# Performance work log

Hardware: AMD Instinct MI355X
Metric: run time of the kernel (lower is better)

The kernel has to match this reference:

```python
import jax, jax.numpy as jnp
import numpy as np

B, S, D, H = 8, 2048, 1024, 128  # batch, seq (== CONTEXT_WINDOW), embed dim, headspace


def setup_inputs() -> dict:
    key = jax.random.key(0)
    ks = jax.random.split(key, 7)
    scale = 1.0 / np.sqrt(D)
    return {
        "x": jax.random.normal(ks[0], (B, S, D), dtype=jnp.float32),
        "Wq": jax.random.normal(ks[1], (D, H), dtype=jnp.float32) * scale,
        "bq": jax.random.normal(ks[2], (H,), dtype=jnp.float32) * 0.01,
        "Wk": jax.random.normal(ks[3], (D, H), dtype=jnp.float32) * scale,
        "bk": jax.random.normal(ks[4], (H,), dtype=jnp.float32) * 0.01,
        "Wv": jax.random.normal(ks[5], (D, H), dtype=jnp.float32) * scale,
        "bv": jax.random.normal(ks[6], (H,), dtype=jnp.float32) * 0.01,
    }


def reference(x, Wq, bq, Wk, bk, Wv, bv):
    # x: [B, S, D]
    embedlen = x.shape[-1]
    q = x @ Wq + bq  # [B, S, H]
    k = x @ Wk + bk  # [B, S, H]
    v = x @ Wv + bv  # [B, S, H]
    # NOTE: original code MULTIPLIES by sqrt(embedlen) (embedlen = full embed dim) --
    # faithful reproduction of the source, not the standard 1/sqrt(head_dim).
    scale = jnp.sqrt(jnp.asarray(embedlen, dtype=x.dtype))
    scores = jnp.einsum("bsh,bth->bst", q, k) * scale  # [B, S, S]
    seqlen = x.shape[1]
    causal = jnp.tril(jnp.ones((seqlen, seqlen), dtype=bool))
    scores = jnp.where(causal, scores, -jnp.inf)
    attn = jax.nn.softmax(scores, axis=-1)
    return jnp.einsum("bst,bth->bsh", attn, v)  # [B, S, H]
```

## Files before the change

kernel.cpp:

```cpp
#include <hip/hip_runtime.h>
#include <math.h>

#define SEQ 2048
#define DIM 1024
#define HD  128
#define NB  8
#define M_TOT (NB * SEQ)

typedef __attribute__((ext_vector_type(8))) short   short8;
typedef __attribute__((ext_vector_type(4))) short   short4v;
typedef __attribute__((ext_vector_type(4))) float   floatx4;

__device__ __forceinline__ unsigned short f2bf(float f) {
    unsigned u = __builtin_bit_cast(unsigned, f);
    u += 0x7FFFu + ((u >> 16) & 1u);
    return (unsigned short)(u >> 16);
}
__device__ __forceinline__ float bf2f(unsigned short h) {
    unsigned u = ((unsigned)h) << 16;
    return __builtin_bit_cast(float, u);
}
__device__ __forceinline__ void async16(const void* g, void* l) {
    __builtin_amdgcn_global_load_lds(
        (const __attribute__((address_space(1))) unsigned int*)g,
        (__attribute__((address_space(3))) unsigned int*)l, 16, 0, 0);
}

#define MFMA16(a, b, c) __builtin_amdgcn_mfma_f32_16x16x32_bf16((a), (b), (c), 0, 0, 0)

__global__ __launch_bounds__(256) void wt_prep(
    const float* __restrict__ Wq, const float* __restrict__ Wk, const float* __restrict__ Wv,
    unsigned short* __restrict__ Wth, unsigned short* __restrict__ Wtl)
{
    int idx = blockIdx.x * 256 + threadIdx.x;
    int k   = idx & 1023;
    int n   = (idx >> 10) & 127;
    int mat = idx >> 17;
    const float* W = (mat == 0) ? Wq : (mat == 1) ? Wk : Wv;
    float v = W[k * HD + n];
    unsigned short hi = f2bf(v);
    Wth[idx] = hi;
    Wtl[idx] = f2bf(v - bf2f(hi));
}

__global__ __launch_bounds__(512, 4) void qkv_fused(
    const float* __restrict__ x,
    const unsigned short* __restrict__ Wth, const unsigned short* __restrict__ Wtl,
    const float* __restrict__ bq, const float* __restrict__ bk, const float* __restrict__ bv,
    unsigned short* __restrict__ Qh, unsigned short* __restrict__ Ql,
    unsigned short* __restrict__ Kh, unsigned short* __restrict__ Kl,
    unsigned short* __restrict__ Vt)
{
    __shared__ short lds[56 * 512];

    const int t    = threadIdx.x;
    const int lane = t & 63;
    const int w    = t >> 6;
    const int lrow = lane & 15;
    const int quad = lane >> 4;

    const int R0 = blockIdx.x * 64;
    const int z  = blockIdx.y;
    const int mh = w & 1;
    const int nh = w >> 1;

    auto stageB = [&](int k0, int qb) {
        #pragma unroll
        for (int i = 0; i < 3; ++i) {
            int f = i * 8 + w;
            if (f < 20) {
                int p   = (f >= 12);
                int ff  = p ? (f - 12) : f;
                int mat = ff >> 2, nfl = ff & 3;
                const unsigned short* src = (p ? Wtl : Wth) + (size_t)mat * (HD * DIM)
                    + (size_t)((z * 4 + nfl) * 16 + lrow) * DIM + k0 + quad * 8;
                async16(src, &lds[(qb * 28 + 8 + f) * 512 + lane * 8]);
            }
        }
    };

    const int arow = t >> 3;
    const int akk  = (t & 7) * 4;
    auto xload = [&](int k0) -> float4 {
        return *(const float4*)&x[(size_t)(R0 + arow) * DIM + k0 + akk];
    };
    auto stageA = [&](float4 xv, int qb) {
        float xf[4] = {xv.x, xv.y, xv.z, xv.w};
        short4v hv, lv;
        #pragma unroll
        for (int j = 0; j < 4; ++j) {
            unsigned short h = f2bf(xf[j]);
            hv[j] = (short)h;
            lv[j] = (short)f2bf(xf[j] - bf2f(h));
        }
        int mi = arow >> 4, lr = arow & 15, qd = akk >> 3, el = akk & 7;
        int base = (qb * 28 + mi * 2) * 512 + (qd * 16 + lr) * 8 + el;
        *(short4v*)&lds[base]       = hv;
        *(short4v*)&lds[base + 512] = lv;
    };

    floatx4 acc[2][3];
    const floatx4 zf = {0.f, 0.f, 0.f, 0.f};
    #pragma unroll
    for (int mi2 = 0; mi2 < 2; ++mi2)
        #pragma unroll
        for (int c = 0; c < 3; ++c) acc[mi2][c] = zf;

    auto compute = [&](int qb) {
        short8 a[2][2];
        #pragma unroll
        for (int mi2 = 0; mi2 < 2; ++mi2)
            #pragma unroll
            for (int p = 0; p < 2; ++p)
                a[mi2][p] = *(short8*)&lds[(qb * 28 + (mh * 2 + mi2) * 2 + p) * 512 + lane * 8];

        short8 bhq = *(short8*)&lds[(qb * 28 + 8 +  0 + nh) * 512 + lane * 8];
        short8 bhk = *(short8*)&lds[(qb * 28 + 8 +  4 + nh) * 512 + lane * 8];
        short8 bhv = *(short8*)&lds[(qb * 28 + 8 +  8 + nh) * 512 + lane * 8];
        short8 blq = *(short8*)&lds[(qb * 28 + 20 + 0 + nh) * 512 + lane * 8];
        short8 blk = *(short8*)&lds[(qb * 28 + 20 + 4 + nh) * 512 + lane * 8];

        #pragma unroll
        for (int mi2 = 0; mi2 < 2; ++mi2) {
            acc[mi2][0] = MFMA16(a[mi2][0], bhq, acc[mi2][0]);
            acc[mi2][1] = MFMA16(a[mi2][0], bhk, acc[mi2][1]);
            acc[mi2][2] = MFMA16(a[mi2][0], bhv, acc[mi2][2]);
            acc[mi2][0] = MFMA16(a[mi2][1], bhq, acc[mi2][0]);
            acc[mi2][1] = MFMA16(a[mi2][1], bhk, acc[mi2][1]);
            acc[mi2][0] = MFMA16(a[mi2][0], blq, acc[mi2][0]);
            acc[mi2][1] = MFMA16(a[mi2][0], blk, acc[mi2][1]);
        }
    };

    stageB(0, 0);
    stageA(xload(0), 0);
    float4 xn0 = xload(32);
    float4 xn1 = xload(64);

    for (int it = 0; it < 32; ++it) {
        __syncthreads();
        const int k0 = it * 32;
        const int q  = it & 1;

        if (it < 31) {
            stageB(k0 + 32, q ^ 1);
            stageA(xn0, q ^ 1);
            xn0 = xn1;
            int kx = (k0 + 96 <= DIM - 32) ? (k0 + 96) : (DIM - 32);
            xn1 = xload(kx);
        }

        compute(q);
    }

    const int col = (z * 4 + nh) * 16 + lrow;
    const float bqv = bq[col], bkv = bk[col], bvv = bv[col];
    #pragma unroll
    for (int mi2 = 0; mi2 < 2; ++mi2) {
        #pragma unroll
        for (int reg = 0; reg < 4; ++reg) {
            int gm = R0 + (mh * 2 + mi2) * 16 + quad * 4 + reg;
            float vq = (acc[mi2][0][reg] + bqv) * 32.0f;
            unsigned short h = f2bf(vq);
            Qh[(size_t)gm * HD + col] = h;
            Ql[(size_t)gm * HD + col] = f2bf(vq - bf2f(h));
            float vk = acc[mi2][1][reg] + bkv;
            h = f2bf(vk);
            Kh[(size_t)gm * HD + col] = h;
            Kl[(size_t)gm * HD + col] = f2bf(vk - bf2f(h));
            float vv = acc[mi2][2][reg] + bvv;
            int b = gm >> 11, s = gm & 2047;
            Vt[((size_t)b * HD + col) * SEQ + s] = f2bf(vv);
        }
    }
}

__global__ __launch_bounds__(256) void flash_attn(
    const unsigned short* __restrict__ Qh, const unsigned short* __restrict__ Ql,
    const unsigned short* __restrict__ Kh, const unsigned short* __restrict__ Kl,
    const unsigned short* __restrict__ Vt, float* __restrict__ out,
    float* __restrict__ Opart, float* __restrict__ ML, int split)
{
    __shared__ short lds[52 * 512];

    const int t    = threadIdx.x;
    const int lane = t & 63;
    const int w    = t >> 6;
    const int lrow = lane & 15;
    const int quad = lane >> 4;

    const int idx = blockIdx.x;
    const int b   = idx & 7;
    const int h   = split ? ((idx >> 3) & 1) : 0;
    const int s   = split ? (63 - (idx >> 4)) : (63 - (idx >> 3));
    const int T   = s + 1;
    const int Th  = (T + 1) >> 1;
    const int t0  = split ? (h ? Th : 0) : 0;
    const int t1  = split ? (h ? T : Th) : T;

    if (split && t0 >= t1) {
        float* op = Opart + (size_t)idx * 4096;
        for (int i = t; i < 4096; i += 256) op[i] = 0.0f;
        if (t < 32) { ML[(idx * 32 + t) * 2] = -1e30f; ML[(idx * 32 + t) * 2 + 1] = 0.0f; }
        return;
    }

    const int mh = w & 1;
    const int kh = w >> 1;
    const int R  = s * 32 + mh * 16;

    const size_t kbase = (size_t)b * SEQ * HD;
    const size_t vbase = (size_t)b * HD * SEQ;

    short8 qf[4][2];
    #pragma unroll
    for (int kc = 0; kc < 4; ++kc) {
        size_t off = kbase + (size_t)(R + lrow) * HD + kc * 32 + quad * 8;
        qf[kc][0] = *(const short8*)(Qh + off);
        qf[kc][1] = *(const short8*)(Ql + off);
    }

    auto stage = [&](int it, int qb) {
        const int j0 = it * 32;
        #pragma unroll
        for (int i = 0; i < 6; ++i) {
            int id = w * 6 + i;
            const unsigned short* src;
            if (id < 16) {
                int nt = id >> 3, kc = (id >> 1) & 3, p = id & 1;
                src = (p ? Kl : Kh) + kbase
                    + (size_t)(j0 + nt * 16 + lrow) * HD + kc * 32 + quad * 8;
            } else {
                int df = id - 16;
                src = Vt + vbase + (size_t)(df * 16 + lrow) * SEQ + j0 + quad * 8;
            }
            async16(src, &lds[(qb * 24 + id) * 512 + lane * 8]);
        }
    };

    const floatx4 zf = {0.f, 0.f, 0.f, 0.f};
    floatx4 accO[8];
    #pragma unroll
    for (int i = 0; i < 8; ++i) accO[i] = zf;
    float m_[4] = {-1e30f, -1e30f, -1e30f, -1e30f};
    float l_[4] = {0.f, 0.f, 0.f, 0.f};

    {
        short8 z8 = {0, 0, 0, 0, 0, 0, 0, 0};
        *(short8*)&lds[(48 + w) * 512 + lane * 8] = z8;
    }

    stage(t0, 0);

    for (int it = t0; it < t1; ++it) {
        const int q = (it - t0) & 1;
        __syncthreads();
        if (it + 1 < t1) stage(it + 1, q ^ 1);
        const int j0 = it * 32;

        floatx4 S = zf;
        #pragma unroll
        for (int kc = 0; kc < 4; ++kc) {
            short8 khf = *(short8*)&lds[(q * 24 + kh * 8 + kc * 2 + 0) * 512 + lane * 8];
            short8 klf = *(short8*)&lds[(q * 24 + kh * 8 + kc * 2 + 1) * 512 + lane * 8];
            S = MFMA16(qf[kc][0], khf, S);
            S = MFMA16(qf[kc][0], klf, S);
            S = MFMA16(qf[kc][1], khf, S);
        }
        if (j0 + kh * 16 + 15 > R) {
            int key = j0 + kh * 16 + lrow;
            #pragma unroll
            for (int reg = 0; reg < 4; ++reg)
                if (key > R + quad * 4 + reg) S[reg] = -INFINITY;
        }
        float alpha[4];
        #pragma unroll
        for (int reg = 0; reg < 4; ++reg) {
            float mx = S[reg];
            #pragma unroll
            for (int hh = 1; hh < 16; hh <<= 1) mx = fmaxf(mx, __shfl_xor(mx, hh));
            float mnew = fmaxf(fmaxf(m_[reg], mx), -1e30f);
            alpha[reg] = __expf(m_[reg] - mnew);
            m_[reg] = mnew;
            float p0 = __expf(S[reg] - mnew);
            S[reg] = p0;
            float ls = p0;
            #pragma unroll
            for (int hh = 1; hh < 16; hh <<= 1) ls += __shfl_xor(ls, hh);
            l_[reg] = l_[reg] * alpha[reg] + ls;
        }
        #pragma unroll
        for (int i = 0; i < 8; ++i)
            #pragma unroll
            for (int reg = 0; reg < 4; ++reg) accO[i][reg] *= alpha[reg];

        #pragma unroll
        for (int reg = 0; reg < 4; ++reg) {
            int kloc = kh * 16 + lrow;
            int jj = kloc & 7, q2 = (kloc >> 3) & 3;
            int lane2 = (quad * 4 + reg) + (q2 << 4);
            lds[(48 + w) * 512 + lane2 * 8 + jj] = (short)f2bf(S[reg]);
        }
        short8 pf = *(short8*)&lds[(48 + w) * 512 + lane * 8];
        #pragma unroll
        for (int df = 0; df < 8; ++df) {
            short8 vf = *(short8*)&lds[(q * 24 + 16 + df) * 512 + lane * 8];
            accO[df] = MFMA16(pf, vf, accO[df]);
        }
    }

    __syncthreads();
    float* fl   = (float*)lds;
    float* Obuf = fl;
    float* mlb  = fl + 4096;
    if (lrow == 0) {
        #pragma unroll
        for (int reg = 0; reg < 4; ++reg) {
            int row = quad * 4 + reg;
            mlb[((kh * 2 + mh) * 16 + row) * 2 + 0] = m_[reg];
            mlb[((kh * 2 + mh) * 16 + row) * 2 + 1] = l_[reg];
        }
    }
    __syncthreads();
    float myw[4], Mrow[4], Drow[4];
    #pragma unroll
    for (int reg = 0; reg < 4; ++reg) {
        int row = quad * 4 + reg;
        float mo  = mlb[(((1 - kh) * 2 + mh) * 16 + row) * 2 + 0];
        float lo_ = mlb[(((1 - kh) * 2 + mh) * 16 + row) * 2 + 1];
        float M = fmaxf(m_[reg], mo);
        float d = l_[reg] * __expf(m_[reg] - M) + lo_ * __expf(mo - M);
        Mrow[reg] = M; Drow[reg] = d;
        myw[reg] = split ? __expf(m_[reg] - M) : (__expf(m_[reg] - M) / d);
    }
    if (kh == 0) {
        #pragma unroll
        for (int df = 0; df < 8; ++df)
            #pragma unroll
            for (int reg = 0; reg < 4; ++reg)
                Obuf[(mh * 16 + quad * 4 + reg) * 128 + df * 16 + lrow] =
                    accO[df][reg] * myw[reg];
    }
    __syncthreads();
    if (kh == 1) {
        if (split) {
            float* op = Opart + (size_t)idx * 4096;
            #pragma unroll
            for (int df = 0; df < 8; ++df) {
                #pragma unroll
                for (int reg = 0; reg < 4; ++reg) {
                    int row = mh * 16 + quad * 4 + reg;
                    op[row * 128 + df * 16 + lrow] =
                        Obuf[row * 128 + df * 16 + lrow] + accO[df][reg] * myw[reg];
                }
            }
            if (lrow == 0) {
                #pragma unroll
                for (int reg = 0; reg < 4; ++reg) {
                    int row = mh * 16 + quad * 4 + reg;
                    ML[(idx * 32 + row) * 2 + 0] = Mrow[reg];
                    ML[(idx * 32 + row) * 2 + 1] = Drow[reg];
                }
            }
        } else {
            #pragma unroll
            for (int df = 0; df < 8; ++df) {
                #pragma unroll
                for (int reg = 0; reg < 4; ++reg) {
                    float v = Obuf[(mh * 16 + quad * 4 + reg) * 128 + df * 16 + lrow]
                            + accO[df][reg] * myw[reg];
                    size_t o = ((size_t)(b * SEQ + R + quad * 4 + reg)) * HD + df * 16 + lrow;
                    out[o] = v;
                }
            }
        }
    }
}

__global__ __launch_bounds__(256) void splitk_merge(
    const float* __restrict__ Opart, const float* __restrict__ ML,
    float* __restrict__ out)
{
    int tid = blockIdx.x * 256 + threadIdx.x;
    int row = tid >> 5, c4 = tid & 31;
    int b = row >> 11, r = row & 2047, s = r >> 5, rr = r & 31;
    int i0 = ((63 - s) << 4) + b;
    int i1 = i0 + 8;
    float m0 = ML[(i0 * 32 + rr) * 2], l0 = ML[(i0 * 32 + rr) * 2 + 1];
    float m1 = ML[(i1 * 32 + rr) * 2], l1 = ML[(i1 * 32 + rr) * 2 + 1];
    float M  = fmaxf(m0, m1);
    float w0 = __expf(m0 - M), w1 = __expf(m1 - M);
    float inv = 1.0f / (w0 * l0 + w1 * l1);
    float4 a  = *(const float4*)&Opart[((size_t)i0 * 32 + rr) * 128 + c4 * 4];
    float4 bb = *(const float4*)&Opart[((size_t)i1 * 32 + rr) * 128 + c4 * 4];
    float4 o;
    o.x = (w0 * a.x + w1 * bb.x) * inv;
    o.y = (w0 * a.y + w1 * bb.y) * inv;
    o.z = (w0 * a.z + w1 * bb.z) * inv;
    o.w = (w0 * a.w + w1 * bb.w) * inv;
    *(float4*)&out[(size_t)row * 128 + c4 * 4] = o;
}

extern "C" void kernel_launch(void* const* d_in, const int* in_sizes, int n_in,
                              void* d_out, int out_size, void* d_ws, size_t ws_size,
                              hipStream_t stream) {
    const float* x  = (const float*)d_in[0];
    const float* Wq = (const float*)d_in[1];
    const float* bq = (const float*)d_in[2];
    const float* Wk = (const float*)d_in[3];
    const float* bk = (const float*)d_in[4];
    const float* Wv = (const float*)d_in[5];
    const float* bv = (const float*)d_in[6];
    float* out = (float*)d_out;

    unsigned short* Qh  = (unsigned short*)d_ws;
    unsigned short* Ql  = Qh  + (size_t)M_TOT * HD;
    unsigned short* Kh  = Ql  + (size_t)M_TOT * HD;
    unsigned short* Kl  = Kh  + (size_t)M_TOT * HD;
    unsigned short* Vt  = Kl  + (size_t)M_TOT * HD;
    unsigned short* Wth = Vt  + (size_t)M_TOT * HD;
    unsigned short* Wtl = Wth + (size_t)3 * HD * DIM;
    float* Opart = (float*)(Wtl + (size_t)3 * HD * DIM);
    float* ML    = Opart + (size_t)1024 * 32 * 128;

    const size_t need = 22544384ULL + 16777216ULL + 262144ULL;
    const int split = (ws_size >= need) ? 1 : 0;

    wt_prep<<<(3 * HD * DIM) / 256, 256, 0, stream>>>(Wq, Wk, Wv, Wth, Wtl);
    qkv_fused<<<dim3(256, 2), 512, 0, stream>>>(x, Wth, Wtl, bq, bk, bv, Qh, Ql, Kh, Kl, Vt);
    flash_attn<<<split ? 1024 : 512, 256, 0, stream>>>(Qh, Ql, Kh, Kl, Vt, out, Opart, ML, split);
    if (split) splitk_merge<<<2048, 256, 0, stream>>>(Opart, ML, out);
}
```

Baseline: 223.0 us.

## Use lazy softmax rescaling and defer row-sum reduction in attention loop

Rescaling of the running max and accumulator is now skipped whenever the new tile max stays within a threshold of the old max across the whole wavefront, so exponentials use a stale max. Per-lane partial sums replace the per-iteration shuffle reduction of the row sum, which is reduced once after the loop. Global source pointers and LDS P-scatter addresses are also precomputed outside the loop. This cuts shuffles and multiplies in the inner loop at the cost of a wave-wide vote and larger unnormalized exponent values.

```diff
diff --git a/kernel.cpp b/kernel.cpp
--- a/kernel.cpp
+++ b/kernel.cpp
@@ -220,21 +220,28 @@
         qf[kc][1] = *(const short8*)(Ql + off);
     }
 
+    const unsigned short* gsrc[6];
+    int gstep[6];
+    #pragma unroll
+    for (int i = 0; i < 6; ++i) {
+        int id = w * 6 + i;
+        if (id < 16) {
+            int nt = id >> 3, kc = (id >> 1) & 3, p = id & 1;
+            gsrc[i] = (p ? Kl : Kh) + kbase
+                + (size_t)(nt * 16 + lrow) * HD + kc * 32 + quad * 8;
+            gstep[i] = 32 * HD;
+        } else {
+            int df = id - 16;
+            gsrc[i] = Vt + vbase + (size_t)(df * 16 + lrow) * SEQ + quad * 8;
+            gstep[i] = 32;
+        }
+    }
     auto stage = [&](int it, int qb) {
-        const int j0 = it * 32;
         #pragma unroll
         for (int i = 0; i < 6; ++i) {
             int id = w * 6 + i;
-            const unsigned short* src;
-            if (id < 16) {
-                int nt = id >> 3, kc = (id >> 1) & 3, p = id & 1;
-                src = (p ? Kl : Kh) + kbase
-                    + (size_t)(j0 + nt * 16 + lrow) * HD + kc * 32 + quad * 8;
-            } else {
-                int df = id - 16;
-                src = Vt + vbase + (size_t)(df * 16 + lrow) * SEQ + j0 + quad * 8;
-            }
-            async16(src, &lds[(qb * 24 + id) * 512 + lane * 8]);
+            async16(gsrc[i] + (size_t)it * gstep[i],
+                    &lds[(qb * 24 + id) * 512 + lane * 8]);
         }
     };
 
@@ -243,11 +250,21 @@
     #pragma unroll
     for (int i = 0; i < 8; ++i) accO[i] = zf;
     float m_[4] = {-1e30f, -1e30f, -1e30f, -1e30f};
-    float l_[4] = {0.f, 0.f, 0.f, 0.f};
+    float sl[4] = {0.f, 0.f, 0.f, 0.f};
 
     {
         short8 z8 = {0, 0, 0, 0, 0, 0, 0, 0};
         *(short8*)&lds[(48 + w) * 512 + lane * 8] = z8;
+    }
+    int paddr[4];
+    {
+        int kloc = kh * 16 + lrow;
+        int jj = kloc & 7, q2 = (kloc >> 3) & 3;
+        #pragma unroll
+        for (int reg = 0; reg < 4; ++reg) {
+            int lane2 = (quad * 4 + reg) + (q2 << 4);
+            paddr[reg] = (48 + w) * 512 + lane2 * 8 + jj;
+        }
     }
 
     stage(t0, 0);
@@ -273,40 +290,58 @@
             for (int reg = 0; reg < 4; ++reg)
                 if (key > R + quad * 4 + reg) S[reg] = -INFINITY;
         }
-        float alpha[4];
+        float mx[4];
         #pragma unroll
         for (int reg = 0; reg < 4; ++reg) {
-            float mx = S[reg];
-            #pragma unroll
-            for (int hh = 1; hh < 16; hh <<= 1) mx = fmaxf(mx, __shfl_xor(mx, hh));
-            float mnew = fmaxf(fmaxf(m_[reg], mx), -1e30f);
-            alpha[reg] = __expf(m_[reg] - mnew);
-            m_[reg] = mnew;
-            float p0 = __expf(S[reg] - mnew);
-            S[reg] = p0;
-            float ls = p0;
-            #pragma unroll
-            for (int hh = 1; hh < 16; hh <<= 1) ls += __shfl_xor(ls, hh);
-            l_[reg] = l_[reg] * alpha[reg] + ls;
-        }
-        #pragma unroll
-        for (int i = 0; i < 8; ++i)
-            #pragma unroll
-            for (int reg = 0; reg < 4; ++reg) accO[i][reg] *= alpha[reg];
-
-        #pragma unroll
-        for (int reg = 0; reg < 4; ++reg) {
-            int kloc = kh * 16 + lrow;
-            int jj = kloc & 7, q2 = (kloc >> 3) & 3;
-            int lane2 = (quad * 4 + reg) + (q2 << 4);
-            lds[(48 + w) * 512 + lane2 * 8 + jj] = (short)f2bf(S[reg]);
-        }
+            float m = S[reg];
+            #pragma unroll
+            for (int hh = 1; hh < 16; hh <<= 1) m = fmaxf(m, __shfl_xor(m, hh));
+            mx[reg] = m;
+        }
+        bool ok = (mx[0] <= m_[0] + 8.0f) & (mx[1] <= m_[1] + 8.0f)
+                & (mx[2] <= m_[2] + 8.0f) & (mx[3] <= m_[3] + 8.0f);
+        if (__all(ok)) {
+            #pragma unroll
+            for (int reg = 0; reg < 4; ++reg) {
+                float p = __expf(S[reg] - m_[reg]);
+                S[reg] = p;
+                sl[reg] += p;
+            }
+        } else {
+            float alpha[4];
+            #pragma unroll
+            for (int reg = 0; reg < 4; ++reg) {
+                float mnew = fmaxf(m_[reg], mx[reg]);
+                alpha[reg] = __expf(m_[reg] - mnew);
+                m_[reg] = mnew;
+                float p = __expf(S[reg] - mnew);
+                S[reg] = p;
+                sl[reg] = sl[reg] * alpha[reg] + p;
+            }
+            #pragma unroll
+            for (int i = 0; i < 8; ++i)
+                #pragma unroll
+                for (int reg = 0; reg < 4; ++reg) accO[i][reg] *= alpha[reg];
+        }
+
+        #pragma unroll
+        for (int reg = 0; reg < 4; ++reg)
+            lds[paddr[reg]] = (short)f2bf(S[reg]);
         short8 pf = *(short8*)&lds[(48 + w) * 512 + lane * 8];
         #pragma unroll
         for (int df = 0; df < 8; ++df) {
             short8 vf = *(short8*)&lds[(q * 24 + 16 + df) * 512 + lane * 8];
             accO[df] = MFMA16(pf, vf, accO[df]);
         }
+    }
+
+    float l_[4];
+    #pragma unroll
+    for (int reg = 0; reg < 4; ++reg) {
+        float ls = sl[reg];
+        #pragma unroll
+        for (int hh = 1; hh < 16; hh <<= 1) ls += __shfl_xor(ls, hh);
+        l_[reg] = ls;
     }
 
     __syncthreads();
```

After: 214.3 us, median of 2. -3.9%, faster.
